# Kernel tuning notes

Measured on AMD Instinct MI355X. Metric: run time of the kernel, lower is better.

The kernel has to match this reference:

```python
import jax, jax.numpy as jnp
import numpy as np

D_SCALED = 8  # adaptive pool output spatial size


def setup_inputs() -> dict:
    key = jax.random.key(0)
    ks = jax.random.split(key, 5)
    b, t, c, h, w = 8, 16, 64, 56, 56
    d_t = 16
    d_in = D_SCALED * D_SCALED  # 64
    d_out = d_t * 2             # 32
    return {
        "x": jax.random.normal(ks[0], (b, t, c, h, w), dtype=jnp.float32),
        "Wq": jax.random.normal(ks[1], (d_in, d_out), dtype=jnp.float32) * 0.001,
        "bq": jax.random.normal(ks[2], (d_out,), dtype=jnp.float32) * 0.001,
        "Wk": jax.random.normal(ks[3], (d_in, d_out), dtype=jnp.float32) * 0.001,
        "bk": jax.random.normal(ks[4], (d_out,), dtype=jnp.float32) * 0.001,
    }


def reference(x, Wq, bq, Wk, bk):
    b, t, c, h, w = x.shape
    ds = D_SCALED
    # shift_x: [b, c, t, h, w]
    shift = jnp.transpose(x, (0, 2, 1, 3, 4))
    # AdaptiveAvgPool3d((None, ds, ds)): h,w divide evenly -> reshape-mean
    pooled = shift.reshape(b, c, t, ds, h // ds, ds, w // ds).mean(axis=(4, 6))
    flat = pooled.reshape(b * c, t, ds * ds)          # [bc, t, ds*ds]
    q = flat @ Wq + bq                                # [bc, t, 2*d_t]
    k = flat @ Wk + bk                                # [bc, t, 2*d_t]
    att = jnp.einsum('ntd,nsd->nts', q, k) / np.sqrt(t).astype(jnp.float32)
    att = jax.nn.softmax(att, axis=-1)                # [bc, t, t]
    v = shift.reshape(b * c, t, h * w)                # [bc, t, h*w]
    out = jnp.einsum('nts,nsv->ntv', att, v)          # [bc, t, h*w]
    out = out.reshape(b, c, t, h, w)
    return jnp.transpose(out, (0, 2, 1, 3, 4))        # [b, t, c, h, w]
```

## Files before the change

### kernel.cpp

```cpp
#include <hip/hip_runtime.h>
#include <math.h>

#define B  8
#define T  16
#define C  64
#define H  56
#define W  56
#define HW (H*W)
#define HW4 (HW/4)
#define CHUNK 196
#define NCHUNK 4
#define DIN 64
#define DOUT 32
#define BC (B*C)

__global__ __launch_bounds__(1024, 8) void fused_kernel(const float* __restrict__ x,
                                                        const float* __restrict__ Wq,
                                                        const float* __restrict__ bq,
                                                        const float* __restrict__ Wk,
                                                        const float* __restrict__ bk,
                                                        float* __restrict__ out) {
    __shared__ float xs[16 * (CHUNK * 4)];
    __shared__ float part[1024];
    __shared__ float pooled_s[T * DIN];
    __shared__ float qs[T * 33];
    __shared__ float ksh[T * 33];
    __shared__ float att_s[T * T];
    __shared__ float att_tr[T * T];

    const int n = blockIdx.x;
    const int tid = threadIdx.x;
    const int b = n >> 6;
    const int c = n & 63;

    const float4* x4 = (const float4*)x;
    float4* o4 = (float4*)out;
    float4* xs4 = (float4*)xs;
    const size_t base = ((size_t)(b * T) * C + c) * HW4;
    const size_t tstr = (size_t)C * HW4;

    #pragma unroll 1
    for (int g = 0; g < NCHUNK; ++g) {
        for (int i = tid; i < 16 * CHUNK; i += 1024) {
            const int s   = i / CHUNK;
            const int off = i - s * CHUNK;
            xs4[i] = x4[base + (size_t)s * tstr + g * CHUNK + off];
        }
        __syncthreads();
        {
            const int q  = tid >> 8;
            const int wi = tid & 255;
            const int sl = wi >> 4;
            const int w8 = wi & 15;
            const int wrow = w8 >> 3;
            const int wcol = w8 & 7;
            const int r0 = 2 * q;
            const int nr = (q < 3) ? 2 : 1;
            float s = 0.f;
            for (int dr = 0; dr < nr; ++dr) {
                const int row = wrow * 7 + r0 + dr;
                const int fbase = sl * (CHUNK * 4) + row * W + wcol * 7;
                #pragma unroll
                for (int j = 0; j < 7; ++j) s += xs[fbase + j];
            }
            part[q * 256 + wi] = s;
        }
        __syncthreads();
        if (tid < 256) {
            const int sl = tid >> 4;
            const int w8 = tid & 15;
            const float v = part[tid] + part[tid + 256] + part[tid + 512] + part[tid + 768];
            pooled_s[sl * DIN + g * 16 + w8] = v * (1.0f / 49.0f);
        }
        __syncthreads();
    }

    if (tid < T * DOUT) {
        const int t = tid >> 5;
        const int d = tid & 31;
        float sq = bq[d];
        float sk = bk[d];
        #pragma unroll 8
        for (int kk = 0; kk < DIN; ++kk) {
            const float f = pooled_s[t * DIN + kk];
            sq = fmaf(f, Wq[kk * DOUT + d], sq);
            sk = fmaf(f, Wk[kk * DOUT + d], sk);
        }
        qs[t * 33 + d] = sq;
        ksh[t * 33 + d] = sk;
    }
    __syncthreads();

    if (tid < T * T) {
        const int tt = tid >> 4;
        const int ss = tid & 15;
        float s = 0.f;
        #pragma unroll
        for (int d = 0; d < DOUT; ++d) s = fmaf(qs[tt * 33 + d], ksh[ss * 33 + d], s);
        att_s[tid] = s * 0.25f;
    }
    __syncthreads();

    if (tid < T) {
        const int r = tid;
        float m = -INFINITY;
        #pragma unroll
        for (int s = 0; s < T; ++s) m = fmaxf(m, att_s[r * T + s]);
        float e[T];
        float sum = 0.f;
        #pragma unroll
        for (int s = 0; s < T; ++s) { e[s] = __expf(att_s[r * T + s] - m); sum += e[s]; }
        const float inv = 1.0f / sum;
        #pragma unroll
        for (int s = 0; s < T; ++s) att_tr[s * T + r] = e[s] * inv;
    }
    __syncthreads();

    #pragma unroll 1
    for (int g = 0; g < NCHUNK; ++g) {
        for (int i = tid; i < 16 * CHUNK; i += 1024) {
            const int s   = i / CHUNK;
            const int off = i - s * CHUNK;
            xs4[i] = x4[base + (size_t)s * tstr + g * CHUNK + off];
        }
        __syncthreads();
        for (int i = tid; i < 16 * CHUNK; i += 1024) {
            const int t   = i / CHUNK;
            const int col = i - t * CHUNK;
            float4 a = make_float4(0.f, 0.f, 0.f, 0.f);
            #pragma unroll 4
            for (int s = 0; s < T; ++s) {
                const float w = att_tr[s * T + t];
                const float4 xv = xs4[s * CHUNK + col];
                a.x = fmaf(w, xv.x, a.x);
                a.y = fmaf(w, xv.y, a.y);
                a.z = fmaf(w, xv.z, a.z);
                a.w = fmaf(w, xv.w, a.w);
            }
            o4[base + (size_t)t * tstr + g * CHUNK + col] = a;
        }
        __syncthreads();
    }
}

extern "C" void kernel_launch(void* const* d_in, const int* in_sizes, int n_in,
                              void* d_out, int out_size, void* d_ws, size_t ws_size,
                              hipStream_t stream) {
    const float* x  = (const float*)d_in[0];
    const float* Wq = (const float*)d_in[1];
    const float* bq = (const float*)d_in[2];
    const float* Wk = (const float*)d_in[3];
    const float* bk = (const float*)d_in[4];
    float* out = (float*)d_out;

    fused_kernel<<<dim3(BC), dim3(1024), 0, stream>>>(x, Wq, bq, Wk, bk, out);
}
```

Before: 208.4 us.

## Prefetch next x chunk into registers while computing current chunk

Replaces the synchronous global-to-shared chunk loads with a register double-buffer. Each thread issues global loads for chunk g+1 right after committing chunk g to shared memory, so memory latency overlaps the pooling and attention-apply compute. The first chunk of the second pass is also issued before the q/k/softmax phase, hiding that latency behind the small attention math. This costs about 16 extra VGPRs per thread, which could reduce occupancy for the 1024-thread blocks.

Measured after the change: 220.4 us. +5.7%, slower.

```diff
diff --git a/kernel.cpp b/kernel.cpp
--- a/kernel.cpp
+++ b/kernel.cpp
@@ -10,6 +10,7 @@
 #define HW4 (HW/4)
 #define CHUNK 196
 #define NCHUNK 4
+#define CELEM (16*CHUNK)
 #define DIN 64
 #define DOUT 32
 #define BC (B*C)
@@ -20,7 +21,7 @@
                                                         const float* __restrict__ Wk,
                                                         const float* __restrict__ bk,
                                                         float* __restrict__ out) {
-    __shared__ float xs[16 * (CHUNK * 4)];
+    __shared__ float xs[CELEM * 4];
     __shared__ float part[1024];
     __shared__ float pooled_s[T * DIN];
     __shared__ float qs[T * 33];
@@ -39,14 +40,37 @@
     const size_t base = ((size_t)(b * T) * C + c) * HW4;
     const size_t tstr = (size_t)C * HW4;
 
+    const int i0 = tid;
+    const int i1 = tid + 1024;
+    const int i2 = tid + 2048;
+    const int i3 = tid + 3072;
+    const int s0 = i0 / CHUNK, f0 = i0 - s0 * CHUNK;
+    const int s1 = i1 / CHUNK, f1 = i1 - s1 * CHUNK;
+    const int s2 = i2 / CHUNK, f2 = i2 - s2 * CHUNK;
+    const int s3 = i3 / CHUNK, f3 = i3 - s3 * CHUNK;
+
+    float4 r0, r1, r2, r3;
+
+    auto issue = [&](int g) {
+        const int gc = g * CHUNK;
+        r0 = x4[base + (size_t)s0 * tstr + gc + f0];
+        r1 = x4[base + (size_t)s1 * tstr + gc + f1];
+        r2 = x4[base + (size_t)s2 * tstr + gc + f2];
+        if (tid < 64) r3 = x4[base + (size_t)s3 * tstr + gc + f3];
+    };
+    auto commit = [&]() {
+        xs4[i0] = r0;
+        xs4[i1] = r1;
+        xs4[i2] = r2;
+        if (tid < 64) xs4[i3] = r3;
+    };
+
+    issue(0);
     #pragma unroll 1
     for (int g = 0; g < NCHUNK; ++g) {
-        for (int i = tid; i < 16 * CHUNK; i += 1024) {
-            const int s   = i / CHUNK;
-            const int off = i - s * CHUNK;
-            xs4[i] = x4[base + (size_t)s * tstr + g * CHUNK + off];
-        }
-        __syncthreads();
+        commit();
+        __syncthreads();
+        if (g + 1 < NCHUNK) issue(g + 1);
         {
             const int q  = tid >> 8;
             const int wi = tid & 255;
@@ -54,11 +78,11 @@
             const int w8 = wi & 15;
             const int wrow = w8 >> 3;
             const int wcol = w8 & 7;
-            const int r0 = 2 * q;
+            const int r0i = 2 * q;
             const int nr = (q < 3) ? 2 : 1;
             float s = 0.f;
             for (int dr = 0; dr < nr; ++dr) {
-                const int row = wrow * 7 + r0 + dr;
+                const int row = wrow * 7 + r0i + dr;
                 const int fbase = sl * (CHUNK * 4) + row * W + wcol * 7;
                 #pragma unroll
                 for (int j = 0; j < 7; ++j) s += xs[fbase + j];
@@ -72,8 +96,10 @@
             const float v = part[tid] + part[tid + 256] + part[tid + 512] + part[tid + 768];
             pooled_s[sl * DIN + g * 16 + w8] = v * (1.0f / 49.0f);
         }
-        __syncthreads();
-    }
+    }
+    __syncthreads();
+
+    issue(0);
 
     if (tid < T * DOUT) {
         const int t = tid >> 5;
@@ -118,26 +144,44 @@
 
     #pragma unroll 1
     for (int g = 0; g < NCHUNK; ++g) {
-        for (int i = tid; i < 16 * CHUNK; i += 1024) {
-            const int s   = i / CHUNK;
-            const int off = i - s * CHUNK;
-            xs4[i] = x4[base + (size_t)s * tstr + g * CHUNK + off];
-        }
-        __syncthreads();
-        for (int i = tid; i < 16 * CHUNK; i += 1024) {
-            const int t   = i / CHUNK;
-            const int col = i - t * CHUNK;
-            float4 a = make_float4(0.f, 0.f, 0.f, 0.f);
-            #pragma unroll 4
-            for (int s = 0; s < T; ++s) {
-                const float w = att_tr[s * T + t];
-                const float4 xv = xs4[s * CHUNK + col];
-                a.x = fmaf(w, xv.x, a.x);
-                a.y = fmaf(w, xv.y, a.y);
-                a.z = fmaf(w, xv.z, a.z);
-                a.w = fmaf(w, xv.w, a.w);
+        commit();
+        __syncthreads();
+        if (g + 1 < NCHUNK) issue(g + 1);
+        {
+            const int gc = g * CHUNK;
+            #pragma unroll
+            for (int k = 0; k < 3; ++k) {
+                const int i   = tid + k * 1024;
+                const int t   = i / CHUNK;
+                const int col = i - t * CHUNK;
+                float4 a = make_float4(0.f, 0.f, 0.f, 0.f);
+                #pragma unroll 4
+                for (int s = 0; s < T; ++s) {
+                    const float w = att_tr[s * T + t];
+                    const float4 xv = xs4[s * CHUNK + col];
+                    a.x = fmaf(w, xv.x, a.x);
+                    a.y = fmaf(w, xv.y, a.y);
+                    a.z = fmaf(w, xv.z, a.z);
+                    a.w = fmaf(w, xv.w, a.w);
+                }
+                o4[base + (size_t)t * tstr + gc + col] = a;
             }
-            o4[base + (size_t)t * tstr + g * CHUNK + col] = a;
+            if (tid < 64) {
+                const int i   = tid + 3072;
+                const int t   = i / CHUNK;
+                const int col = i - t * CHUNK;
+                float4 a = make_float4(0.f, 0.f, 0.f, 0.f);
+                #pragma unroll 4
+                for (int s = 0; s < T; ++s) {
+                    const float w = att_tr[s * T + t];
+                    const float4 xv = xs4[s * CHUNK + col];
+                    a.x = fmaf(w, xv.x, a.x);
+                    a.y = fmaf(w, xv.y, a.y);
+                    a.z = fmaf(w, xv.z, a.z);
+                    a.w = fmaf(w, xv.w, a.w);
+                }
+                o4[base + (size_t)t * tstr + gc + col] = a;
+            }
         }
         __syncthreads();
     }
```
